# Performance work log

Measured on AMD Instinct MI355X. Metric: run time of the kernel, lower is better.

## Reference

```python
import jax, jax.numpy as jnp
import numpy as np

H, D, MAX_SEQ = 8, 512, 2048
DH = D // H
B, S = 2, 2048


def setup_inputs() -> dict:
    key = jax.random.key(0)
    ks = jax.random.split(key, 12)
    sc = 1.0 / np.sqrt(D)
    inp = {
        'q_in': jax.random.normal(ks[0], (B, S, D), jnp.float32),
        'k_in': jax.random.normal(ks[1], (B, S, D), jnp.float32),
        'v_in': jax.random.normal(ks[2], (B, S, D), jnp.float32),
        # causal look-ahead mask: 1.0 where attention is disallowed (j > i)
        'mask': jnp.triu(jnp.ones((S, S), jnp.float32), k=1)[None, None, :, :],
        'Wq': jax.random.normal(ks[3], (D, D), jnp.float32) * sc,
        'bq': jnp.zeros((D,), jnp.float32),
        'Wk': jax.random.normal(ks[4], (D, D), jnp.float32) * sc,
        'bk': jnp.zeros((D,), jnp.float32),
        'Wv': jax.random.normal(ks[5], (D, D), jnp.float32) * sc,
        'bv': jnp.zeros((D,), jnp.float32),
        'Wo': jax.random.normal(ks[6], (D, D), jnp.float32) * sc,
        'bo': jnp.zeros((D,), jnp.float32),
        'E': jax.random.normal(ks[7], (MAX_SEQ, DH), jnp.float32) * sc,
    }
    return inp


def _split_heads(x):
    b, s, _ = x.shape
    return x.reshape(b, s, H, DH).transpose(0, 2, 1, 3)  # [B,H,S,DH]


def _qe_masking(qe):
    # qe: [B,H,Lq,M]; keep entry (l, j) only when j >= M-1-l (valid rel positions)
    lq, m = qe.shape[-2], qe.shape[-1]
    keep = jnp.arange(m)[None, :] >= (m - 1 - jnp.arange(lq))[:, None]
    return qe * keep.astype(qe.dtype)


def _skewing(qe, len_q, len_k):
    # pad 1 on the left of last dim, reshape to swap last two dims, drop first row
    b, h, lq, m = qe.shape
    padded = jnp.pad(qe, ((0, 0), (0, 0), (0, 0), (1, 0)))  # [B,H,Lq,M+1]
    reshaped = padded.reshape(b, h, m + 1, lq)
    srel = reshaped[:, :, 1:, :]  # [B,H,M,Lq] == [B,H,Lq,Lq] since M==Lq here
    if len_k > len_q:
        srel = jnp.pad(srel, ((0, 0), (0, 0), (0, 0), (0, len_k - len_q)))
    elif len_k < len_q:
        srel = srel[:, :, :, :len_k]
    return srel


def reference(q_in, k_in, v_in, mask, Wq, bq, Wk, bk, Wv, bv, Wo, bo, E):
    q = _split_heads(q_in @ Wq + bq)  # [B,H,Lq,DH]
    k = _split_heads(k_in @ Wk + bk)  # [B,H,Lk,DH]
    v = _split_heads(v_in @ Wv + bv)
    len_q, len_k = q.shape[2], k.shape[2]
    start = max(0, MAX_SEQ - len_q)
    e = E[start:, :]  # [M,DH], M = len_q
    qe = jnp.einsum('bhld,md->bhlm', q, e)
    qe = _qe_masking(qe)
    srel = _skewing(qe, len_q, len_k)
    logits = (jnp.einsum('bhld,bhmd->bhlm', q, k) + srel) / np.sqrt(DH)
    logits = logits + mask * (-1e9)
    attn = jax.nn.softmax(logits, axis=-1)  # [B,H,Lq,Lk]
    out = jnp.einsum('bhlm,bhmd->bhld', attn, v)
    out = out.transpose(0, 2, 1, 3).reshape(q_in.shape[0], -1, D)
    out = out @ Wo + bo
    return out, attn
```

## Files before the change

### kernel.cpp

```cpp
#include <hip/hip_runtime.h>
#include <hip/hip_bf16.h>


namespace {
constexpr int kS  = 2048;
constexpr int kD  = 512;
constexpr int kH  = 8;
constexpr int kDH = 64;
constexpr int kB  = 2;

typedef __attribute__((ext_vector_type(8))) short short8;
typedef __attribute__((ext_vector_type(4))) float f32x4;

constexpr int kKl = 0;
constexpr int kVl = 8192;
constexpr int kEl = 16384;
constexpr int kPf = 26624;
constexpr int kLs = 30976;
}

__device__ __forceinline__ f32x4 mfma16(short8 a, short8 b, f32x4 c) {
    return __builtin_amdgcn_mfma_f32_16x16x32_bf16(a, b, c, 0, 0, 0);
}

__device__ __forceinline__ short bfbits(float f) {
    __hip_bfloat16 h = __float2bfloat16(f);
    return *reinterpret_cast<short*>(&h);
}

__global__ __launch_bounds__(256)
void convw_kernel(const float* __restrict__ Wq, const float* __restrict__ Wk,
                  const float* __restrict__ Wv, const float* __restrict__ Wo,
                  const float* __restrict__ E,
                  ushort* __restrict__ Wqt, ushort* __restrict__ Wkt,
                  ushort* __restrict__ Wvt, ushort* __restrict__ Wot,
                  ushort* __restrict__ eb)
{
    const int z = blockIdx.z;
    const int tid = threadIdx.x;
    if (z == 4) {
        const int idx = ((blockIdx.y * 8 + blockIdx.x) * 256 + tid) * 8;
        const float4 x = *reinterpret_cast<const float4*>(E + idx);
        const float4 y = *reinterpret_cast<const float4*>(E + idx + 4);
        short8 r;
        r[0] = bfbits(x.x); r[1] = bfbits(x.y); r[2] = bfbits(x.z); r[3] = bfbits(x.w);
        r[4] = bfbits(y.x); r[5] = bfbits(y.y); r[6] = bfbits(y.z); r[7] = bfbits(y.w);
        *reinterpret_cast<short8*>(eb + idx) = r;
        return;
    }
    const float* W = (z == 0) ? Wq : (z == 1) ? Wk : (z == 2) ? Wv : Wo;
    ushort* Wt = (z == 0) ? Wqt : (z == 1) ? Wkt : (z == 2) ? Wvt : Wot;

    __shared__ float Ws[64][65];
    const int k0 = blockIdx.x * 64;
    const int c0 = blockIdx.y * 64;
    const int cc = tid & 63;
    const int rq = tid >> 6;
    #pragma unroll
    for (int ii = 0; ii < 16; ++ii) {
        const int r = ii * 4 + rq;
        Ws[r][cc] = W[(size_t)(k0 + r) * kD + c0 + cc];
    }
    __syncthreads();
    #pragma unroll
    for (int ii = 0; ii < 16; ++ii) {
        const int r = ii * 4 + rq;
        Wt[(size_t)(c0 + r) * kD + k0 + cc] = (ushort)bfbits(Ws[cc][r]);
    }
}

template<int MODE, bool AF32>
__device__ __forceinline__
void gemm_lds_core(char* lds, const void* __restrict__ Av,
                   const ushort* __restrict__ Wt,
                   const float* __restrict__ bias, void* __restrict__ out)
{
    char* As = lds;
    char* Ws = lds + 8192;

    const int tid  = threadIdx.x;
    const int w    = tid >> 6;
    const int lane = tid & 63;
    const int g    = lane >> 4;
    const int n15  = lane & 15;
    const int r0   = blockIdx.x * 64;
    const int c0   = blockIdx.y * 32;

    f32x4 acc0 = {0.f, 0.f, 0.f, 0.f};
    f32x4 acc1 = {0.f, 0.f, 0.f, 0.f};

    const int rA  = w * 16 + n15;
    const int swA = (n15 & 7) << 4;
    const int swB = (n15 & 7) << 4;

    for (int kb = 0; kb < 8; ++kb) {
        const int k0 = kb * 64;
        __syncthreads();
        #pragma unroll
        for (int hh = 0; hh < 2; ++hh) {
            const int c = tid + hh * 256;
            const int row = c >> 3, i = c & 7;
            short8 v;
            if (AF32) {
                const float* src = (const float*)Av + (size_t)(r0 + row) * kD + k0 + i * 8;
                const float4 x = *reinterpret_cast<const float4*>(src);
                const float4 y = *reinterpret_cast<const float4*>(src + 4);
                v[0] = bfbits(x.x); v[1] = bfbits(x.y); v[2] = bfbits(x.z); v[3] = bfbits(x.w);
                v[4] = bfbits(y.x); v[5] = bfbits(y.y); v[6] = bfbits(y.z); v[7] = bfbits(y.w);
            } else {
                v = *reinterpret_cast<const short8*>(
                    (const ushort*)Av + (size_t)(r0 + row) * kD + k0 + i * 8);
            }
            *reinterpret_cast<short8*>(As + row * 128 + ((i * 16) ^ ((row & 7) << 4))) = v;
        }
        {
            const int crow = tid >> 3, i = tid & 7;
            const short8 v = *reinterpret_cast<const short8*>(
                Wt + (size_t)(c0 + crow) * kD + k0 + i * 8);
            *reinterpret_cast<short8*>(Ws + crow * 128 + ((i * 16) ^ ((crow & 7) << 4))) = v;
        }
        __syncthreads();

        #pragma unroll
        for (int ks = 0; ks < 2; ++ks) {
            const int bo = ks * 64 + g * 16;
            const short8 a  = *reinterpret_cast<const short8*>(As + rA * 128 + (bo ^ swA));
            const short8 b0 = *reinterpret_cast<const short8*>(Ws + n15 * 128 + (bo ^ swB));
            const short8 b1 = *reinterpret_cast<const short8*>(Ws + (16 + n15) * 128 + (bo ^ swB));
            acc0 = mfma16(a, b0, acc0);
            acc1 = mfma16(a, b1, acc1);
        }
    }

    #pragma unroll
    for (int cg = 0; cg < 2; ++cg) {
        const f32x4 acc = cg ? acc1 : acc0;
        const int c = c0 + cg * 16 + n15;
        const float bb = bias[c];
        const int h = c >> 6, d = c & (kDH - 1);
        #pragma unroll
        for (int j = 0; j < 4; ++j) {
            const int r = r0 + w * 16 + g * 4 + j;
            const float val = acc[j] + bb;
            const int b = r >> 11, s2 = r & (kS - 1);
            if (MODE == 0) {
                ((float*)out)[(size_t)r * kD + c] = val;
            } else if (MODE == 1) {
                ((ushort*)out)[((size_t)(b * kH + h) * kS + s2) * kDH + d] = (ushort)bfbits(val);
            } else {
                ((ushort*)out)[((size_t)(b * kH + h) * kDH + d) * kS + s2] = (ushort)bfbits(val);
            }
        }
    }
}

__global__ __launch_bounds__(256)
void gemm_qkv_kernel(const float* __restrict__ q_in, const float* __restrict__ k_in,
                     const float* __restrict__ v_in,
                     const ushort* __restrict__ Wqt, const ushort* __restrict__ Wkt,
                     const ushort* __restrict__ Wvt,
                     const float* __restrict__ bq, const float* __restrict__ bk,
                     const float* __restrict__ bv,
                     ushort* __restrict__ qh, ushort* __restrict__ kh,
                     ushort* __restrict__ vt)
{
    __shared__ __align__(16) char lds[12288];
    const int z = blockIdx.z;
    const float*  A    = (z == 0) ? q_in : (z == 1) ? k_in : v_in;
    const ushort* Wt   = (z == 0) ? Wqt  : (z == 1) ? Wkt  : Wvt;
    const float*  bias = (z == 0) ? bq   : (z == 1) ? bk   : bv;
    void*         out  = (z == 0) ? (void*)qh : (z == 1) ? (void*)kh : (void*)vt;
    if (z == 2) gemm_lds_core<2, true>(lds, A, Wt, bias, out);
    else        gemm_lds_core<1, true>(lds, A, Wt, bias, out);
}

__global__ __launch_bounds__(256)
void gemm_o_kernel(const ushort* __restrict__ ohb, const ushort* __restrict__ Wot,
                   const float* __restrict__ bo, float* __restrict__ out)
{
    __shared__ __align__(16) char lds[12288];
    gemm_lds_core<0, false>(lds, ohb, Wot, bo, out);
}

__global__ __launch_bounds__(256, 4)
void attn_fused_kernel(const ushort* __restrict__ qh, const ushort* __restrict__ khp,
                       const ushort* __restrict__ vt, const ushort* __restrict__ eb,
                       float* __restrict__ attn, ushort* __restrict__ ohb)
{
    __shared__ __align__(16) char smem[31232];
    float* Pf     = (float*)(smem + kPf);
    float* lsum_s = (float*)(smem + kLs);

    const int bh    = blockIdx.x;
    const int strip = 127 - (int)blockIdx.y;
    const int l0    = strip * 16;
    const int tid   = threadIdx.x;
    const int w     = tid >> 6;
    const int lane  = tid & 63;
    const int g     = lane >> 4;
    const int n15   = lane & 15;
    const size_t bhS = (size_t)bh * kS;

    const int T = ((l0 + 15) >> 6) + 1;

    const ushort* qrow = qh + (bhS + l0 + n15) * kDH;
    const short8 aq0 = *reinterpret_cast<const short8*>(qrow + g * 8);
    const short8 aq1 = *reinterpret_cast<const short8*>(qrow + 32 + g * 8);

    int  srcl[4];
    bool condj[4];
    #pragma unroll
    for (int j = 0; j < 4; ++j) {
        const int d = n15 + 15 - (g * 4 + j);
        srcl[j]  = (lane & 48) | (d & 15);
        condj[j] = (d >= 16);
    }

    const int rW = w * 16 + n15;
    const int mS = (n15 & 7) << 4;
    const int b0 = (g * 16) ^ mS;
    const int b1 = (64 + g * 16) ^ mS;

    float lsum[4] = {0.f, 0.f, 0.f, 0.f};
    for (int t = 0; t < T; ++t) {
        const int k0 = t * 64;
        const int m_lo = 2032 + k0 - l0;
        __syncthreads();
        for (int c = tid; c < 512; c += 256) {
            const int row = c >> 3, bi = (c & 7) * 16;
            const short8 v = *reinterpret_cast<const short8*>(
                khp + (bhS + k0 + row) * kDH + (c & 7) * 8);
            *reinterpret_cast<short8*>(smem + kKl + row * 128 + (bi ^ ((row & 7) << 4))) = v;
        }
        for (int c = tid; c < 640; c += 256) {
            const int row = c >> 3, bi = (c & 7) * 16;
            const int er = min(m_lo + row, kS - 1);
            const short8 v = *reinterpret_cast<const short8*>(
                eb + (size_t)er * kDH + (c & 7) * 8);
            *reinterpret_cast<short8*>(smem + kEl + row * 128 + (bi ^ ((row & 7) << 4))) = v;
        }
        __syncthreads();

        f32x4 s4 = {0.f, 0.f, 0.f, 0.f};
        s4 = mfma16(aq0, *reinterpret_cast<const short8*>(smem + kKl + rW * 128 + b0), s4);
        s4 = mfma16(aq1, *reinterpret_cast<const short8*>(smem + kKl + rW * 128 + b1), s4);
        f32x4 qe2[2];
        #pragma unroll
        for (int q2 = 0; q2 < 2; ++q2) {
            const int rE = w * 16 + q2 * 16 + n15;
            f32x4 acc = {0.f, 0.f, 0.f, 0.f};
            acc = mfma16(aq0, *reinterpret_cast<const short8*>(smem + kEl + rE * 128 + b0), acc);
            qe2[q2] = mfma16(aq1, *reinterpret_cast<const short8*>(smem + kEl + rE * 128 + b1), acc);
        }
        #pragma unroll
        for (int j = 0; j < 4; ++j) {
            const float sh0 = __shfl(qe2[0][j], srcl[j]);
            const float sh1 = __shfl(qe2[1][j], srcl[j]);
            const float rel = condj[j] ? sh1 : sh0;
            float v = (s4[j] + rel) * 0.125f;
            v = fminf(v, 60.f);
            const bool keep = (k0 + w * 16 + n15 <= l0 + g * 4 + j);
            lsum[j] += keep ? __expf(v) : 0.f;
        }
    }
    #pragma unroll
    for (int j = 0; j < 4; ++j) {
        float s = lsum[j];
        #pragma unroll
        for (int off = 1; off < 16; off <<= 1) s += __shfl_xor(s, off);
        if (n15 == 0) lsum_s[w * 16 + g * 4 + j] = s;
    }
    __syncthreads();

    float linv[4];
    #pragma unroll
    for (int j = 0; j < 4; ++j) {
        const int r = g * 4 + j;
        linv[j] = 1.f / (lsum_s[r] + lsum_s[16 + r] + lsum_s[32 + r] + lsum_s[48 + r]);
    }

    f32x4 o = {0.f, 0.f, 0.f, 0.f};
    const int srow = tid >> 4;
    const int scol = (tid & 15) * 4;

    for (int t = 0; t < 32; ++t) {
        const int k0 = t * 64;
        if (t >= T) {
            const f32x4 z = {0.f, 0.f, 0.f, 0.f};
            __builtin_nontemporal_store(
                z, reinterpret_cast<f32x4*>(attn + (bhS + l0 + srow) * kS + k0 + scol));
            continue;
        }
        const int m_lo = 2032 + k0 - l0;
        __syncthreads();
        for (int c = tid; c < 512; c += 256) {
            const int row = c >> 3, bi = (c & 7) * 16;
            const short8 v = *reinterpret_cast<const short8*>(
                khp + (bhS + k0 + row) * kDH + (c & 7) * 8);
            *reinterpret_cast<short8*>(smem + kKl + row * 128 + (bi ^ ((row & 7) << 4))) = v;
        }
        for (int c = tid; c < 512; c += 256) {
            const int row = c >> 3, bi = (c & 7) * 16;
            const short8 v = *reinterpret_cast<const short8*>(
                vt + ((size_t)bh * kDH + row) * kS + k0 + (c & 7) * 8);
            *reinterpret_cast<short8*>(smem + kVl + row * 128 + (bi ^ ((row & 7) << 4))) = v;
        }
        for (int c = tid; c < 640; c += 256) {
            const int row = c >> 3, bi = (c & 7) * 16;
            const int er = min(m_lo + row, kS - 1);
            const short8 v = *reinterpret_cast<const short8*>(
                eb + (size_t)er * kDH + (c & 7) * 8);
            *reinterpret_cast<short8*>(smem + kEl + row * 128 + (bi ^ ((row & 7) << 4))) = v;
        }
        __syncthreads();

        f32x4 s4 = {0.f, 0.f, 0.f, 0.f};
        s4 = mfma16(aq0, *reinterpret_cast<const short8*>(smem + kKl + rW * 128 + b0), s4);
        s4 = mfma16(aq1, *reinterpret_cast<const short8*>(smem + kKl + rW * 128 + b1), s4);
        f32x4 qe2[2];
        #pragma unroll
        for (int q2 = 0; q2 < 2; ++q2) {
            const int rE = w * 16 + q2 * 16 + n15;
            f32x4 acc = {0.f, 0.f, 0.f, 0.f};
            acc = mfma16(aq0, *reinterpret_cast<const short8*>(smem + kEl + rE * 128 + b0), acc);
            qe2[q2] = mfma16(aq1, *reinterpret_cast<const short8*>(smem + kEl + rE * 128 + b1), acc);
        }
        #pragma unroll
        for (int j = 0; j < 4; ++j) {
            const float sh0 = __shfl(qe2[0][j], srcl[j]);
            const float sh1 = __shfl(qe2[1][j], srcl[j]);
            const float rel = condj[j] ? sh1 : sh0;
            float v = (s4[j] + rel) * 0.125f;
            v = fminf(v, 60.f);
            const bool keep = (k0 + w * 16 + n15 <= l0 + g * 4 + j);
            const float pe = keep ? __expf(v) * linv[j] : 0.f;
            Pf[(g * 4 + j) * 68 + w * 16 + n15] = pe;
        }
        __syncthreads();

        const f32x4 pv4 = *reinterpret_cast<const f32x4*>(Pf + srow * 68 + scol);
        __builtin_nontemporal_store(
            pv4, reinterpret_cast<f32x4*>(attn + (bhS + l0 + srow) * kS + k0 + scol));

        const f32x4 plo0 = *reinterpret_cast<const f32x4*>(Pf + n15 * 68 + g * 8);
        const f32x4 phi0 = *reinterpret_cast<const f32x4*>(Pf + n15 * 68 + g * 8 + 4);
        const f32x4 plo1 = *reinterpret_cast<const f32x4*>(Pf + n15 * 68 + 32 + g * 8);
        const f32x4 phi1 = *reinterpret_cast<const f32x4*>(Pf + n15 * 68 + 32 + g * 8 + 4);
        short8 pa0, pa1;
        #pragma unroll
        for (int i = 0; i < 4; ++i) {
            pa0[i] = bfbits(plo0[i]); pa0[4 + i] = bfbits(phi0[i]);
            pa1[i] = bfbits(plo1[i]); pa1[4 + i] = bfbits(phi1[i]);
        }
        o = mfma16(pa0, *reinterpret_cast<const short8*>(smem + kVl + rW * 128 + b0), o);
        o = mfma16(pa1, *reinterpret_cast<const short8*>(smem + kVl + rW * 128 + b1), o);
    }

    const int b = bh >> 3, h = bh & 7;
    #pragma unroll
    for (int j = 0; j < 4; ++j)
        ohb[((size_t)b * kS + l0 + g * 4 + j) * kD + h * kDH + w * 16 + n15] =
            (ushort)bfbits(o[j]);
}

extern "C" void kernel_launch(void* const* d_in, const int* in_sizes, int n_in,
                              void* d_out, int out_size, void* d_ws, size_t ws_size,
                              hipStream_t stream)
{
    const float* q_in = (const float*)d_in[0];
    const float* k_in = (const float*)d_in[1];
    const float* v_in = (const float*)d_in[2];
    const float* Wq = (const float*)d_in[4];
    const float* bq = (const float*)d_in[5];
    const float* Wk = (const float*)d_in[6];
    const float* bk = (const float*)d_in[7];
    const float* Wv = (const float*)d_in[8];
    const float* bv = (const float*)d_in[9];
    const float* Wo = (const float*)d_in[10];
    const float* bo = (const float*)d_in[11];
    const float* E  = (const float*)d_in[12];

    float* out  = (float*)d_out;
    float* attn = (float*)d_out + (size_t)kB * kS * kD;

    ushort* qh  = (ushort*)d_ws;
    ushort* kh  = qh  + 2097152;
    ushort* vt  = kh  + 2097152;
    ushort* ohb = vt  + 2097152;
    ushort* eb  = ohb + 2097152;
    ushort* Wqt = eb  + 131072;
    ushort* Wkt = Wqt + 262144;
    ushort* Wvt = Wkt + 262144;
    ushort* Wot = Wvt + 262144;

    convw_kernel<<<dim3(8, 8, 5), 256, 0, stream>>>(Wq, Wk, Wv, Wo, E,
                                                    Wqt, Wkt, Wvt, Wot, eb);
    gemm_qkv_kernel<<<dim3(64, 16, 3), 256, 0, stream>>>(q_in, k_in, v_in,
                                                         Wqt, Wkt, Wvt,
                                                         bq, bk, bv, qh, kh, vt);
    attn_fused_kernel<<<dim3(16, 128), 256, 0, stream>>>(qh, kh, vt, eb, attn, ohb);
    gemm_o_kernel<<<dim3(64, 16), 256, 0, stream>>>(ohb, Wot, bo, out);
}
```

Baseline: 160.3 us.

## Add two-pass attention kernel spilling unnormalized bf16 probabilities to workspace

Adds a new attention kernel that computes exp(logits) once per causal tile, stores the unnormalized bf16 probabilities to a global workspace, and accumulates row sums. A second loop reloads those tiles to write the normalized attention matrix and to run the P·V MFMAs, with zeros written for fully masked tiles. It drops max-subtraction in favour of clamping logits at 60, removing online rescaling and recomputation of QK/QE. The cost is extra global traffic for the workspace, and the kernel is used only when the workspace is large enough, falling back to the old fused kernel otherwise.

```diff
diff --git a/kernel.cpp b/kernel.cpp
--- a/kernel.cpp
+++ b/kernel.cpp
@@ -10,6 +10,7 @@
 constexpr int kB  = 2;
 
 typedef __attribute__((ext_vector_type(8))) short short8;
+typedef __attribute__((ext_vector_type(4))) short short4v;
 typedef __attribute__((ext_vector_type(4))) float f32x4;
 
 constexpr int kKl = 0;
@@ -17,6 +18,15 @@
 constexpr int kEl = 16384;
 constexpr int kPf = 26624;
 constexpr int kLs = 30976;
+
+constexpr int pKl = 0;
+constexpr int pPl = 8192;
+constexpr int pEl = 8192;
+constexpr int pLs = 18432;
+constexpr int pLi = 18688;
+constexpr int pSz = 18752;
+
+constexpr size_t kPwsElems = (size_t)16 * 2112 * 1024;
 }
 
 __device__ __forceinline__ f32x4 mfma16(short8 a, short8 b, f32x4 c) {
@@ -26,6 +36,11 @@
 __device__ __forceinline__ short bfbits(float f) {
     __hip_bfloat16 h = __float2bfloat16(f);
     return *reinterpret_cast<short*>(&h);
+}
+
+__device__ __forceinline__ float bf2f(short b) {
+    const unsigned u = (unsigned)(unsigned short)b << 16;
+    return __uint_as_float(u);
 }
 
 __global__ __launch_bounds__(256)
@@ -182,6 +197,162 @@
     gemm_lds_core<0, false>(lds, ohb, Wot, bo, out);
 }
 
+__global__ __launch_bounds__(256, 6)
+void attn_ps_kernel(const ushort* __restrict__ qh, const ushort* __restrict__ khp,
+                    const ushort* __restrict__ vt, const ushort* __restrict__ eb,
+                    float* __restrict__ attn, ushort* __restrict__ ohb,
+                    ushort* __restrict__ Pws)
+{
+    __shared__ __align__(16) char smem[pSz];
+    float* lsum_s = (float*)(smem + pLs);
+    float* linv_s = (float*)(smem + pLi);
+
+    const int bh    = blockIdx.x;
+    const int strip = 127 - (int)blockIdx.y;
+    const int l0    = strip * 16;
+    const int tid   = threadIdx.x;
+    const int w     = tid >> 6;
+    const int lane  = tid & 63;
+    const int g     = lane >> 4;
+    const int n15   = lane & 15;
+    const size_t bhS = (size_t)bh * kS;
+
+    const int T = (strip >> 2) + 1;
+
+    const int pa_ = strip >> 2, pb_ = strip & 3;
+    const int pbase = strip + 2 * pa_ * (pa_ - 1) + pa_ * pb_;
+    ushort* Pstrip = Pws + ((size_t)bh * 2112 + pbase) * 1024;
+
+    const ushort* qrow = qh + (bhS + l0 + n15) * kDH;
+    const short8 aq0 = *reinterpret_cast<const short8*>(qrow + g * 8);
+    const short8 aq1 = *reinterpret_cast<const short8*>(qrow + 32 + g * 8);
+
+    int  srcl[4];
+    bool condj[4];
+    #pragma unroll
+    for (int j = 0; j < 4; ++j) {
+        const int d = n15 + 15 - (g * 4 + j);
+        srcl[j]  = (lane & 48) | (d & 15);
+        condj[j] = (d >= 16);
+    }
+
+    const int rW = w * 16 + n15;
+    const int mS = (n15 & 7) << 4;
+    const int b0 = (g * 16) ^ mS;
+    const int b1 = (64 + g * 16) ^ mS;
+    const int pcol = w * 16 + n15;
+
+    float lsum[4] = {0.f, 0.f, 0.f, 0.f};
+    for (int t = 0; t < T; ++t) {
+        const int k0 = t * 64;
+        const int m_lo = 2032 + k0 - l0;
+        __syncthreads();
+        for (int c = tid; c < 512; c += 256) {
+            const int row = c >> 3, bi = (c & 7) * 16;
+            const short8 v = *reinterpret_cast<const short8*>(
+                khp + (bhS + k0 + row) * kDH + (c & 7) * 8);
+            *reinterpret_cast<short8*>(smem + pKl + row * 128 + (bi ^ ((row & 7) << 4))) = v;
+        }
+        for (int c = tid; c < 640; c += 256) {
+            const int row = c >> 3, bi = (c & 7) * 16;
+            const int er = min(m_lo + row, kS - 1);
+            const short8 v = *reinterpret_cast<const short8*>(
+                eb + (size_t)er * kDH + (c & 7) * 8);
+            *reinterpret_cast<short8*>(smem + pEl + row * 128 + (bi ^ ((row & 7) << 4))) = v;
+        }
+        __syncthreads();
+
+        f32x4 s4 = {0.f, 0.f, 0.f, 0.f};
+        s4 = mfma16(aq0, *reinterpret_cast<const short8*>(smem + pKl + rW * 128 + b0), s4);
+        s4 = mfma16(aq1, *reinterpret_cast<const short8*>(smem + pKl + rW * 128 + b1), s4);
+        f32x4 qe2[2];
+        #pragma unroll
+        for (int q2 = 0; q2 < 2; ++q2) {
+            const int rE = w * 16 + q2 * 16 + n15;
+            f32x4 acc = {0.f, 0.f, 0.f, 0.f};
+            acc = mfma16(aq0, *reinterpret_cast<const short8*>(smem + pEl + rE * 128 + b0), acc);
+            qe2[q2] = mfma16(aq1, *reinterpret_cast<const short8*>(smem + pEl + rE * 128 + b1), acc);
+        }
+        ushort* ptile = Pstrip + (size_t)t * 1024;
+        #pragma unroll
+        for (int j = 0; j < 4; ++j) {
+            const float sh0 = __shfl(qe2[0][j], srcl[j]);
+            const float sh1 = __shfl(qe2[1][j], srcl[j]);
+            const float rel = condj[j] ? sh1 : sh0;
+            float v = (s4[j] + rel) * 0.125f;
+            v = fminf(v, 60.f);
+            const bool keep = (k0 + pcol <= l0 + g * 4 + j);
+            const float pe = keep ? __expf(v) : 0.f;
+            const short pb = bfbits(pe);
+            lsum[j] += bf2f(pb);
+            ptile[(g * 4 + j) * 64 + pcol] = (ushort)pb;
+        }
+    }
+    #pragma unroll
+    for (int j = 0; j < 4; ++j) {
+        float s = lsum[j];
+        #pragma unroll
+        for (int off = 1; off < 16; off <<= 1) s += __shfl_xor(s, off);
+        if (n15 == 0) lsum_s[w * 16 + g * 4 + j] = s;
+    }
+    __syncthreads();
+    if (tid < 16)
+        linv_s[tid] = 1.f / (lsum_s[tid] + lsum_s[16 + tid] +
+                             lsum_s[32 + tid] + lsum_s[48 + tid]);
+    __syncthreads();
+
+    f32x4 o = {0.f, 0.f, 0.f, 0.f};
+    const int srow = tid >> 4;
+    const int scol = (tid & 15) * 4;
+    const int sby  = ((tid & 15) * 8) ^ ((srow & 7) << 4);
+
+    for (int t = 0; t < 32; ++t) {
+        const int k0 = t * 64;
+        if (t >= T) {
+            const f32x4 z = {0.f, 0.f, 0.f, 0.f};
+            __builtin_nontemporal_store(
+                z, reinterpret_cast<f32x4*>(attn + (bhS + l0 + srow) * kS + k0 + scol));
+            continue;
+        }
+        __syncthreads();
+        for (int c = tid; c < 512; c += 256) {
+            const int row = c >> 3, bi = (c & 7) * 16;
+            const short8 v = *reinterpret_cast<const short8*>(
+                vt + ((size_t)bh * kDH + row) * kS + k0 + (c & 7) * 8);
+            *reinterpret_cast<short8*>(smem + pKl + row * 128 + (bi ^ ((row & 7) << 4))) = v;
+        }
+        {
+            const short4v pv = *reinterpret_cast<const short4v*>(
+                Pstrip + (size_t)t * 1024 + tid * 4);
+            const int prow = tid >> 4;
+            const int pbyte = (tid & 15) * 8;
+            *reinterpret_cast<short4v*>(
+                smem + pPl + prow * 128 + (pbyte ^ ((prow & 7) << 4))) = pv;
+        }
+        __syncthreads();
+
+        {
+            const short4v pv = *reinterpret_cast<const short4v*>(smem + pPl + srow * 128 + sby);
+            const float li = linv_s[srow];
+            f32x4 o4;
+            #pragma unroll
+            for (int i = 0; i < 4; ++i) o4[i] = bf2f(pv[i]) * li;
+            __builtin_nontemporal_store(
+                o4, reinterpret_cast<f32x4*>(attn + (bhS + l0 + srow) * kS + k0 + scol));
+        }
+        const short8 pa0 = *reinterpret_cast<const short8*>(smem + pPl + n15 * 128 + b0);
+        const short8 pa1 = *reinterpret_cast<const short8*>(smem + pPl + n15 * 128 + b1);
+        o = mfma16(pa0, *reinterpret_cast<const short8*>(smem + pKl + rW * 128 + b0), o);
+        o = mfma16(pa1, *reinterpret_cast<const short8*>(smem + pKl + rW * 128 + b1), o);
+    }
+
+    const int b = bh >> 3, h = bh & 7;
+    #pragma unroll
+    for (int j = 0; j < 4; ++j)
+        ohb[((size_t)b * kS + l0 + g * 4 + j) * kD + h * kDH + w * 16 + n15] =
+            (ushort)bfbits(o[j] * linv_s[g * 4 + j]);
+}
+
 __global__ __launch_bounds__(256, 4)
 void attn_fused_kernel(const ushort* __restrict__ qh, const ushort* __restrict__ khp,
                        const ushort* __restrict__ vt, const ushort* __restrict__ eb,
@@ -392,12 +563,21 @@
     ushort* Wkt = Wqt + 262144;
     ushort* Wvt = Wkt + 262144;
     ushort* Wot = Wvt + 262144;
+    ushort* Pws = Wot + 262144;
+
+    const size_t need = (size_t)((char*)(Pws + kPwsElems) - (char*)d_ws);
 
     convw_kernel<<<dim3(8, 8, 5), 256, 0, stream>>>(Wq, Wk, Wv, Wo, E,
                                                     Wqt, Wkt, Wvt, Wot, eb);
     gemm_qkv_kernel<<<dim3(64, 16, 3), 256, 0, stream>>>(q_in, k_in, v_in,
                                                          Wqt, Wkt, Wvt,
                                                          bq, bk, bv, qh, kh, vt);
-    attn_fused_kernel<<<dim3(16, 128), 256, 0, stream>>>(qh, kh, vt, eb, attn, ohb);
+    if (ws_size >= need) {
+        attn_ps_kernel<<<dim3(16, 128), 256, 0, stream>>>(qh, kh, vt, eb,
+                                                          attn, ohb, Pws);
+    } else {
+        attn_fused_kernel<<<dim3(16, 128), 256, 0, stream>>>(qh, kh, vt, eb,
+                                                             attn, ohb);
+    }
     gemm_o_kernel<<<dim3(64, 16), 256, 0, stream>>>(ohb, Wot, bo, out);
 }
```

Result: faster. 138.8 us (median of 2 runs) (-13.4%).
